# Kernel optimization log

Hardware: AMD Instinct MI355X
Metric: run time of the kernel (lower is better)

The kernel has to match this reference:

```python
import jax, jax.numpy as jnp
import numpy as np

B, T, IN, H, HH, OUT = 512, 512, 6, 64, 128, 8


def setup_inputs() -> dict:
    key = jax.random.key(0)
    ks = jax.random.split(key, 14)
    def lin(k, fan_in, shape):
        s = 1.0 / np.sqrt(fan_in)
        return jax.random.uniform(k, shape, jnp.float32, -s, s)
    return {
        "x": jax.random.normal(ks[0], (B, T, IN), jnp.float32),
        # initial_linear: input_dim -> hidden
        "W_init": lin(ks[1], IN, (IN, H)), "b_init": lin(ks[2], IN, (H,)),
        # vector-field MLP: hidden -> hh -> hh -> hh -> hidden*input
        "W_in": lin(ks[3], H, (H, HH)),  "b_in": lin(ks[4], H, (HH,)),
        "W_h1": lin(ks[5], HH, (HH, HH)), "b_h1": lin(ks[6], HH, (HH,)),
        "W_h2": lin(ks[7], HH, (HH, HH)), "b_h2": lin(ks[8], HH, (HH,)),
        "W_out": lin(ks[9], HH, (HH, H * IN)), "b_out": lin(ks[10], HH, (H * IN,)),
        # final linear: hidden -> output
        "W_fin": lin(ks[11], H, (H, OUT)), "b_fin": lin(ks[12], H, (OUT,)),
    }


def reference(x, W_init, b_init, W_in, b_in, W_h1, b_h1, W_h2, b_h2,
              W_out, b_out, W_fin, b_fin):
    # vector field: f(h) -> (B, H, IN) matrix; dh/dt = f(h) @ dX/dt
    def vf(h, dX):
        z = jax.nn.relu(h @ W_in + b_in)
        z = jax.nn.relu(z @ W_h1 + b_h1)
        z = jax.nn.relu(z @ W_h2 + b_h2)
        A = jnp.tanh(z @ W_out + b_out).reshape(h.shape[0], H, IN)
        return jnp.einsum("bhi,bi->bh", A, dX)

    # h0 from initial value of the path (spline.evaluate(0) == x[:, 0])
    h0 = x[:, 0] @ W_init + b_init  # (B, H)

    # linear interpolation: dX/dt constant on each unit interval
    dX = jnp.swapaxes(x[:, 1:] - x[:, :-1], 0, 1)  # (T-1, B, IN)

    def rk4_step(h, d):
        k1 = vf(h, d)
        k2 = vf(h + 0.5 * k1, d)
        k3 = vf(h + 0.5 * k2, d)
        k4 = vf(h + k3, d)
        h_new = h + (k1 + 2.0 * k2 + 2.0 * k3 + k4) / 6.0
        return h_new, h_new

    _, hs = jax.lax.scan(rk4_step, h0, dX)  # (T-1, B, H)
    hidden = jnp.concatenate([h0[None], hs], axis=0)  # (T, B, H)
    hidden = jnp.swapaxes(hidden, 0, 1)  # (B, T, H)

    # return_sequences=True -> final linear on all steps
    return hidden @ W_fin + b_fin  # (B, T, OUT)
```

## Files before the change

### kernel.cpp

```cpp
#include <hip/hip_runtime.h>
#include <stdint.h>

namespace {

constexpr int B_   = 512;
constexpr int T_   = 512;
constexpr int IN_  = 6;
constexpr int H_   = 64;
constexpr int HH_  = 128;
constexpr int OUT_ = 8;

typedef _Float16 f16x2 __attribute__((ext_vector_type(2)));

__device__ __forceinline__ float dot2f(uint32_t w, uint32_t z, float acc) {
    return __builtin_amdgcn_fdot2(__builtin_bit_cast(f16x2, w),
                                  __builtin_bit_cast(f16x2, z), acc, false);
}

__device__ __forceinline__ uint32_t pack2f(float a, float b) {
    f16x2 p;
    p[0] = (_Float16)a;
    p[1] = (_Float16)b;
    return __builtin_bit_cast(uint32_t, p);
}

__device__ __forceinline__ float pxor1(float v) {
    int y = __builtin_amdgcn_mov_dpp(__builtin_bit_cast(int, v), 0xB1, 0xF, 0xF, true);
    return v + __builtin_bit_cast(float, y);
}

__device__ __forceinline__ float pxor2(float v) {
    int y = __builtin_amdgcn_mov_dpp(__builtin_bit_cast(int, v), 0x4E, 0xF, 0xF, true);
    return v + __builtin_bit_cast(float, y);
}

__device__ __forceinline__ float tanh_fast(float v) {
    float ax = fabsf(v);
    float e  = __expf(2.0f * ax);
    float r  = 1.0f - 2.0f / (e + 1.0f);
    return copysignf(r, v);
}

__global__ __launch_bounds__(256, 2) void cde_kernel(
    const float* __restrict__ x,
    const float* __restrict__ W_init, const float* __restrict__ b_init,
    const float* __restrict__ W_in,   const float* __restrict__ b_in,
    const float* __restrict__ W_h1,   const float* __restrict__ b_h1,
    const float* __restrict__ W_h2,   const float* __restrict__ b_h2,
    const float* __restrict__ W_out,  const float* __restrict__ b_out,
    const float* __restrict__ W_fin,  const float* __restrict__ b_fin,
    float* __restrict__ out)
{
    const int t  = threadIdx.x;
    const int c  = t >> 1;
    const int kh = t & 1;
    const int b  = blockIdx.x;

    __shared__ alignas(16) uint32_t hinu[H_ / 2];
    __shared__ alignas(16) uint32_t zAu[HH_ / 2];
    __shared__ alignas(16) uint32_t zBu[HH_ / 2];
    __shared__ uint32_t w1s[32 * HH_];
    __shared__ float dxs[IN_];
    __shared__ float hbuf[H_];
    __shared__ float wfin_s[H_ * OUT_];
    __shared__ float bfin_s[OUT_];

    uint32_t w2[32], w3[32], w4[96];
    #pragma unroll
    for (int i = 0; i < 32; ++i) {
        int k = kh * 64 + 2 * i;
        w2[i] = pack2f(W_h1[k * HH_ + c], W_h1[(k + 1) * HH_ + c]);
        w3[i] = pack2f(W_h2[k * HH_ + c], W_h2[(k + 1) * HH_ + c]);
    }
    #pragma unroll
    for (int j = 0; j < 3; ++j) {
        const int col = 3 * c + j;
        #pragma unroll
        for (int i = 0; i < 32; ++i) {
            int k = kh * 64 + 2 * i;
            w4[j * 32 + i] = pack2f(W_out[k * 384 + col], W_out[(k + 1) * 384 + col]);
        }
    }
    for (int i = t; i < 32 * HH_; i += 256) {
        int kp = i >> 7, cc = i & 127;
        w1s[i] = pack2f(W_in[(2 * kp) * HH_ + cc], W_in[(2 * kp + 1) * HH_ + cc]);
    }
    for (int i = t; i < H_ * OUT_; i += 256) wfin_s[i] = W_fin[i];
    if (t < OUT_) bfin_s[t] = b_fin[t];

    const float bin_r = b_in[c];
    const float bh1_r = b_h1[c];
    const float bh2_r = b_h2[c];
    float bo[3];
    #pragma unroll
    for (int j = 0; j < 3; ++j) bo[j] = b_out[3 * c + j];
    const int  dbase = (c & 1) * 3;
    const int  r_own = t >> 2;
    const bool wrt   = (t & 3) == 0;

    const size_t xbase = (size_t)b * T_ * IN_;
    const size_t obase = (size_t)b * T_ * OUT_;

    float xa = 0.f, xb = 0.f;
    if (t < IN_) {
        xa = x[xbase + t];
        xb = x[xbase + IN_ + t];
        dxs[t] = xb - xa;
        xa = xb;
        xb = x[xbase + 2 * IN_ + t];
    }

    if (t < H_) {
        float s = b_init[t];
        #pragma unroll
        for (int i = 0; i < IN_; ++i) s += x[xbase + i] * W_init[i * H_ + t];
        hbuf[t] = s;
        ((_Float16*)hinu)[t] = (_Float16)s;
    }
    __syncthreads();

    float h_reg = hbuf[r_own];
    float hacc  = 0.f;

#define OUT_STAGE(TT)                                                          \
    if (t < 64) {                                                              \
        int o_ = t & 7, part_ = t >> 3;                                        \
        float s_ = 0.f;                                                        \
        _Pragma("unroll")                                                      \
        for (int j = 0; j < 8; ++j)                                            \
            s_ += hbuf[part_ * 8 + j] * wfin_s[(part_ * 8 + j) * OUT_ + o_];   \
        s_ += __shfl_xor(s_, 8);                                               \
        s_ += __shfl_xor(s_, 16);                                              \
        s_ += __shfl_xor(s_, 32);                                              \
        if (part_ == 0)                                                        \
            out[obase + (size_t)(TT) * OUT_ + o_] = s_ + bfin_s[o_];           \
    }

    OUT_STAGE(0)

    float dxr[3];

    for (int step = 0; step < T_ - 1; ++step) {
        #pragma unroll
        for (int s4 = 0; s4 < 4; ++s4) {
            if (s4 == 0) {
                #pragma unroll
                for (int j = 0; j < 3; ++j) dxr[j] = dxs[dbase + j];
                if (step > 0) { OUT_STAGE(step) }
            }
            {
                uint32_t hv[16];
                const uint32_t* hp = hinu + kh * 16;
                *(uint4*)&hv[0]  = *(const uint4*)(hp);
                *(uint4*)&hv[4]  = *(const uint4*)(hp + 4);
                *(uint4*)&hv[8]  = *(const uint4*)(hp + 8);
                *(uint4*)&hv[12] = *(const uint4*)(hp + 12);
                const int w1base = (kh * 16) * HH_ + c;
                float a0 = 0.f, a1 = 0.f, a2 = 0.f, a3 = 0.f;
                #pragma unroll
                for (int i = 0; i < 16; ++i) {
                    uint32_t wv = w1s[w1base + i * HH_];
                    if ((i & 3) == 0)      a0 = dot2f(wv, hv[i], a0);
                    else if ((i & 3) == 1) a1 = dot2f(wv, hv[i], a1);
                    else if ((i & 3) == 2) a2 = dot2f(wv, hv[i], a2);
                    else                   a3 = dot2f(wv, hv[i], a3);
                }
                float z = fmaxf(bin_r + pxor1((a0 + a1) + (a2 + a3)), 0.f);
                if (kh == 0) ((_Float16*)zAu)[c] = (_Float16)z;
            }
            __syncthreads();

            {
                uint32_t zv[32];
                const uint32_t* zp = zAu + kh * 32;
                #pragma unroll
                for (int q = 0; q < 8; ++q)
                    *(uint4*)&zv[4 * q] = *(const uint4*)(zp + 4 * q);
                float a0 = 0.f, a1 = 0.f, a2 = 0.f, a3 = 0.f;
                #pragma unroll
                for (int i = 0; i < 32; ++i) {
                    if ((i & 3) == 0)      a0 = dot2f(w2[i], zv[i], a0);
                    else if ((i & 3) == 1) a1 = dot2f(w2[i], zv[i], a1);
                    else if ((i & 3) == 2) a2 = dot2f(w2[i], zv[i], a2);
                    else                   a3 = dot2f(w2[i], zv[i], a3);
                }
                float z = fmaxf(bh1_r + pxor1((a0 + a1) + (a2 + a3)), 0.f);
                if (kh == 0) ((_Float16*)zBu)[c] = (_Float16)z;
            }
            __syncthreads();

            {
                uint32_t zv[32];
                const uint32_t* zp = zBu + kh * 32;
                #pragma unroll
                for (int q = 0; q < 8; ++q)
                    *(uint4*)&zv[4 * q] = *(const uint4*)(zp + 4 * q);
                float a0 = 0.f, a1 = 0.f, a2 = 0.f, a3 = 0.f;
                #pragma unroll
                for (int i = 0; i < 32; ++i) {
                    if ((i & 3) == 0)      a0 = dot2f(w3[i], zv[i], a0);
                    else if ((i & 3) == 1) a1 = dot2f(w3[i], zv[i], a1);
                    else if ((i & 3) == 2) a2 = dot2f(w3[i], zv[i], a2);
                    else                   a3 = dot2f(w3[i], zv[i], a3);
                }
                float z = fmaxf(bh2_r + pxor1((a0 + a1) + (a2 + a3)), 0.f);
                if (kh == 0) ((_Float16*)zAu)[c] = (_Float16)z;
            }
            __syncthreads();

            {
                uint32_t zv[32];
                const uint32_t* zp = zAu + kh * 32;
                #pragma unroll
                for (int q = 0; q < 8; ++q)
                    *(uint4*)&zv[4 * q] = *(const uint4*)(zp + 4 * q);
                float p0 = 0.f, p1 = 0.f, p2 = 0.f, p3 = 0.f, p4 = 0.f, p5 = 0.f;
                #pragma unroll
                for (int i = 0; i < 16; ++i) {
                    uint32_t ze = zv[2 * i], zo = zv[2 * i + 1];
                    p0 = dot2f(w4[2 * i],          ze, p0);
                    p1 = dot2f(w4[2 * i + 1],      zo, p1);
                    p2 = dot2f(w4[32 + 2 * i],     ze, p2);
                    p3 = dot2f(w4[32 + 2 * i + 1], zo, p3);
                    p4 = dot2f(w4[64 + 2 * i],     ze, p4);
                    p5 = dot2f(w4[64 + 2 * i + 1], zo, p5);
                }
                float av0 = bo[0] + pxor1(p0 + p1);
                float av1 = bo[1] + pxor1(p2 + p3);
                float av2 = bo[2] + pxor1(p4 + p5);
                float kvp = tanh_fast(av0) * dxr[0]
                          + tanh_fast(av1) * dxr[1]
                          + tanh_fast(av2) * dxr[2];
                float kv = pxor2(kvp);

                hacc += ((s4 == 1 || s4 == 2) ? 2.0f : 1.0f) * kv;
                float hs;
                if (s4 < 3) {
                    hs = h_reg + ((s4 == 2) ? 1.0f : 0.5f) * kv;
                } else {
                    h_reg += hacc * (1.0f / 6.0f);
                    hacc = 0.f;
                    hs = h_reg;
                }
                if (wrt) {
                    ((_Float16*)hinu)[r_own] = (_Float16)hs;
                    if (s4 == 3) hbuf[r_own] = h_reg;
                }
            }
            if (s4 == 3 && step + 2 < T_ && t < IN_) {
                dxs[t] = xb - xa;
                xa = xb;
                if (step + 3 < T_) xb = x[xbase + (size_t)(step + 3) * IN_ + t];
            }
            __syncthreads();
        }
    }

    OUT_STAGE(T_ - 1)
#undef OUT_STAGE
}

}

extern "C" void kernel_launch(void* const* d_in, const int* in_sizes, int n_in,
                              void* d_out, int out_size, void* d_ws, size_t ws_size,
                              hipStream_t stream) {
    const float* x      = (const float*)d_in[0];
    const float* W_init = (const float*)d_in[1];
    const float* b_init = (const float*)d_in[2];
    const float* W_in   = (const float*)d_in[3];
    const float* b_in   = (const float*)d_in[4];
    const float* W_h1   = (const float*)d_in[5];
    const float* b_h1   = (const float*)d_in[6];
    const float* W_h2   = (const float*)d_in[7];
    const float* b_h2   = (const float*)d_in[8];
    const float* W_out  = (const float*)d_in[9];
    const float* b_out  = (const float*)d_in[10];
    const float* W_fin  = (const float*)d_in[11];
    const float* b_fin  = (const float*)d_in[12];
    float* out = (float*)d_out;

    cde_kernel<<<dim3(B_), dim3(256), 0, stream>>>(
        x, W_init, b_init, W_in, b_in, W_h1, b_h1, W_h2, b_h2,
        W_out, b_out, W_fin, b_fin, out);
}
```

Baseline: 3.229 ms.

## Move hidden-layer weights to padded LDS, keep W_in in registers, disable AGPRs

Moves the W_h1 and W_h2 weight slices out of per-thread registers into padded, row-major LDS tables read with 128-bit loads, and moves W_in from LDS into registers. The goal is to lower VGPR pressure so the 2-blocks-per-CU launch bound fits without spills or AGPR use, and to replace strided scalar LDS reads with vectorized ones. The dot-product chains are rearranged into fewer accumulators that interleave loads with compute, and the W_fin table is padded to 9 columns to reduce bank conflicts. The trade-off is extra LDS traffic for the two 128x128 layers on every RK4 substage, plus longer dependent FMA chains from having fewer accumulators.

```diff
diff --git a/kernel.cpp b/kernel.cpp
--- a/kernel.cpp
+++ b/kernel.cpp
@@ -1,5 +1,15 @@
 #include <hip/hip_runtime.h>
 #include <stdint.h>
+
+#if defined(__has_attribute)
+#if __has_attribute(amdgpu_agpr_alloc)
+#define AGPR0 __attribute__((amdgpu_agpr_alloc(0)))
+#else
+#define AGPR0
+#endif
+#else
+#define AGPR0
+#endif
 
 namespace {
 
@@ -10,6 +20,10 @@
 constexpr int HH_  = 128;
 constexpr int OUT_ = 8;
 
+constexpr int WROW = 36;
+constexpr int WOFF = HH_ * WROW + 16;
+constexpr int WSZ  = WOFF + HH_ * WROW;
+
 typedef _Float16 f16x2 __attribute__((ext_vector_type(2)));
 
 __device__ __forceinline__ float dot2f(uint32_t w, uint32_t z, float acc) {
@@ -28,7 +42,6 @@
     int y = __builtin_amdgcn_mov_dpp(__builtin_bit_cast(int, v), 0xB1, 0xF, 0xF, true);
     return v + __builtin_bit_cast(float, y);
 }
-
 __device__ __forceinline__ float pxor2(float v) {
     int y = __builtin_amdgcn_mov_dpp(__builtin_bit_cast(int, v), 0x4E, 0xF, 0xF, true);
     return v + __builtin_bit_cast(float, y);
@@ -41,7 +54,7 @@
     return copysignf(r, v);
 }
 
-__global__ __launch_bounds__(256, 2) void cde_kernel(
+__global__ AGPR0 __launch_bounds__(256, 2) void cde_kernel(
     const float* __restrict__ x,
     const float* __restrict__ W_init, const float* __restrict__ b_init,
     const float* __restrict__ W_in,   const float* __restrict__ b_in,
@@ -56,21 +69,21 @@
     const int kh = t & 1;
     const int b  = blockIdx.x;
 
+    __shared__ alignas(16) uint32_t w2s[WSZ];
+    __shared__ alignas(16) uint32_t w3s[WSZ];
     __shared__ alignas(16) uint32_t hinu[H_ / 2];
     __shared__ alignas(16) uint32_t zAu[HH_ / 2];
     __shared__ alignas(16) uint32_t zBu[HH_ / 2];
-    __shared__ uint32_t w1s[32 * HH_];
     __shared__ float dxs[IN_];
     __shared__ float hbuf[H_];
-    __shared__ float wfin_s[H_ * OUT_];
+    __shared__ float wfin_s[H_ * 9];
     __shared__ float bfin_s[OUT_];
 
-    uint32_t w2[32], w3[32], w4[96];
+    uint32_t w1[16], w4[96];
     #pragma unroll
-    for (int i = 0; i < 32; ++i) {
-        int k = kh * 64 + 2 * i;
-        w2[i] = pack2f(W_h1[k * HH_ + c], W_h1[(k + 1) * HH_ + c]);
-        w3[i] = pack2f(W_h2[k * HH_ + c], W_h2[(k + 1) * HH_ + c]);
+    for (int i = 0; i < 16; ++i) {
+        int k = kh * 32 + 2 * i;
+        w1[i] = pack2f(W_in[k * HH_ + c], W_in[(k + 1) * HH_ + c]);
     }
     #pragma unroll
     for (int j = 0; j < 3; ++j) {
@@ -81,11 +94,18 @@
             w4[j * 32 + i] = pack2f(W_out[k * 384 + col], W_out[(k + 1) * 384 + col]);
         }
     }
-    for (int i = t; i < 32 * HH_; i += 256) {
-        int kp = i >> 7, cc = i & 127;
-        w1s[i] = pack2f(W_in[(2 * kp) * HH_ + cc], W_in[(2 * kp + 1) * HH_ + cc]);
-    }
-    for (int i = t; i < H_ * OUT_; i += 256) wfin_s[i] = W_fin[i];
+    for (int i = t; i < 2 * HH_ * 32; i += 256) {
+        int khw = i >> 12;
+        int rem = i & 4095;
+        int kp  = rem >> 7;
+        int cc  = rem & 127;
+        int dst = khw * WOFF + cc * WROW + kp;
+        int k   = khw * 64 + 2 * kp;
+        w2s[dst] = pack2f(W_h1[k * HH_ + cc], W_h1[(k + 1) * HH_ + cc]);
+        w3s[dst] = pack2f(W_h2[k * HH_ + cc], W_h2[(k + 1) * HH_ + cc]);
+    }
+    for (int i = t; i < H_ * OUT_; i += 256)
+        wfin_s[(i >> 3) * 9 + (i & 7)] = W_fin[i];
     if (t < OUT_) bfin_s[t] = b_fin[t];
 
     const float bin_r = b_in[c];
@@ -95,8 +115,11 @@
     #pragma unroll
     for (int j = 0; j < 3; ++j) bo[j] = b_out[3 * c + j];
     const int  dbase = (c & 1) * 3;
-    const int  r_own = t >> 2;
+    const int  r_own = c >> 1;
     const bool wrt   = (t & 3) == 0;
+
+    const uint32_t* wp2 = w2s + kh * WOFF + c * WROW;
+    const uint32_t* wp3 = w3s + kh * WOFF + c * WROW;
 
     const size_t xbase = (size_t)b * T_ * IN_;
     const size_t obase = (size_t)b * T_ * OUT_;
@@ -128,7 +151,7 @@
         float s_ = 0.f;                                                        \
         _Pragma("unroll")                                                      \
         for (int j = 0; j < 8; ++j)                                            \
-            s_ += hbuf[part_ * 8 + j] * wfin_s[(part_ * 8 + j) * OUT_ + o_];   \
+            s_ += hbuf[part_ * 8 + j] * wfin_s[(part_ * 8 + j) * 9 + o_];      \
         s_ += __shfl_xor(s_, 8);                                               \
         s_ += __shfl_xor(s_, 16);                                              \
         s_ += __shfl_xor(s_, 32);                                              \
@@ -149,88 +172,147 @@
                 if (step > 0) { OUT_STAGE(step) }
             }
             {
-                uint32_t hv[16];
                 const uint32_t* hp = hinu + kh * 16;
-                *(uint4*)&hv[0]  = *(const uint4*)(hp);
-                *(uint4*)&hv[4]  = *(const uint4*)(hp + 4);
-                *(uint4*)&hv[8]  = *(const uint4*)(hp + 8);
-                *(uint4*)&hv[12] = *(const uint4*)(hp + 12);
-                const int w1base = (kh * 16) * HH_ + c;
-                float a0 = 0.f, a1 = 0.f, a2 = 0.f, a3 = 0.f;
-                #pragma unroll
-                for (int i = 0; i < 16; ++i) {
-                    uint32_t wv = w1s[w1base + i * HH_];
-                    if ((i & 3) == 0)      a0 = dot2f(wv, hv[i], a0);
-                    else if ((i & 3) == 1) a1 = dot2f(wv, hv[i], a1);
-                    else if ((i & 3) == 2) a2 = dot2f(wv, hv[i], a2);
-                    else                   a3 = dot2f(wv, hv[i], a3);
-                }
-                float z = fmaxf(bin_r + pxor1((a0 + a1) + (a2 + a3)), 0.f);
+                uint4 q0 = *reinterpret_cast<const uint4*>(hp);
+                uint4 q1 = *reinterpret_cast<const uint4*>(hp + 4);
+                uint4 q2 = *reinterpret_cast<const uint4*>(hp + 8);
+                uint4 q3 = *reinterpret_cast<const uint4*>(hp + 12);
+                float a = 0.f, d = 0.f;
+                #pragma unroll
+                for (int m = 0; m < 4; ++m) {
+                    a = dot2f(w1[m],      (&q0.x)[m], a);
+                    d = dot2f(w1[4 + m],  (&q1.x)[m], d);
+                    a = dot2f(w1[8 + m],  (&q2.x)[m], a);
+                    d = dot2f(w1[12 + m], (&q3.x)[m], d);
+                }
+                float z = fmaxf(bin_r + pxor1(a + d), 0.f);
                 if (kh == 0) ((_Float16*)zAu)[c] = (_Float16)z;
             }
             __syncthreads();
 
             {
-                uint32_t zv[32];
                 const uint32_t* zp = zAu + kh * 32;
-                #pragma unroll
-                for (int q = 0; q < 8; ++q)
-                    *(uint4*)&zv[4 * q] = *(const uint4*)(zp + 4 * q);
-                float a0 = 0.f, a1 = 0.f, a2 = 0.f, a3 = 0.f;
-                #pragma unroll
-                for (int i = 0; i < 32; ++i) {
-                    if ((i & 3) == 0)      a0 = dot2f(w2[i], zv[i], a0);
-                    else if ((i & 3) == 1) a1 = dot2f(w2[i], zv[i], a1);
-                    else if ((i & 3) == 2) a2 = dot2f(w2[i], zv[i], a2);
-                    else                   a3 = dot2f(w2[i], zv[i], a3);
-                }
-                float z = fmaxf(bh1_r + pxor1((a0 + a1) + (a2 + a3)), 0.f);
+                uint4 z0 = *reinterpret_cast<const uint4*>(zp);
+                uint4 z1 = *reinterpret_cast<const uint4*>(zp + 4);
+                uint4 wa = *reinterpret_cast<const uint4*>(wp2);
+                uint4 wb = *reinterpret_cast<const uint4*>(wp2 + 4);
+                float a = 0.f, d = 0.f;
+                #pragma unroll
+                for (int m = 0; m < 4; ++m) {
+                    a = dot2f((&wa.x)[m], (&z0.x)[m], a);
+                    d = dot2f((&wb.x)[m], (&z1.x)[m], d);
+                }
+                uint4 z2 = *reinterpret_cast<const uint4*>(zp + 8);
+                uint4 z3 = *reinterpret_cast<const uint4*>(zp + 12);
+                uint4 wc = *reinterpret_cast<const uint4*>(wp2 + 8);
+                uint4 wd = *reinterpret_cast<const uint4*>(wp2 + 12);
+                #pragma unroll
+                for (int m = 0; m < 4; ++m) {
+                    a = dot2f((&wc.x)[m], (&z2.x)[m], a);
+                    d = dot2f((&wd.x)[m], (&z3.x)[m], d);
+                }
+                uint4 z4 = *reinterpret_cast<const uint4*>(zp + 16);
+                uint4 z5 = *reinterpret_cast<const uint4*>(zp + 20);
+                uint4 we = *reinterpret_cast<const uint4*>(wp2 + 16);
+                uint4 wf = *reinterpret_cast<const uint4*>(wp2 + 20);
+                #pragma unroll
+                for (int m = 0; m < 4; ++m) {
+                    a = dot2f((&we.x)[m], (&z4.x)[m], a);
+                    d = dot2f((&wf.x)[m], (&z5.x)[m], d);
+                }
+                uint4 z6 = *reinterpret_cast<const uint4*>(zp + 24);
+                uint4 z7 = *reinterpret_cast<const uint4*>(zp + 28);
+                uint4 wg = *reinterpret_cast<const uint4*>(wp2 + 24);
+                uint4 wh = *reinterpret_cast<const uint4*>(wp2 + 28);
+                #pragma unroll
+                for (int m = 0; m < 4; ++m) {
+                    a = dot2f((&wg.x)[m], (&z6.x)[m], a);
+                    d = dot2f((&wh.x)[m], (&z7.x)[m], d);
+                }
+                float z = fmaxf(bh1_r + pxor1(a + d), 0.f);
                 if (kh == 0) ((_Float16*)zBu)[c] = (_Float16)z;
             }
             __syncthreads();
 
             {
-                uint32_t zv[32];
                 const uint32_t* zp = zBu + kh * 32;
-                #pragma unroll
-                for (int q = 0; q < 8; ++q)
-                    *(uint4*)&zv[4 * q] = *(const uint4*)(zp + 4 * q);
-                float a0 = 0.f, a1 = 0.f, a2 = 0.f, a3 = 0.f;
-                #pragma unroll
-                for (int i = 0; i < 32; ++i) {
-                    if ((i & 3) == 0)      a0 = dot2f(w3[i], zv[i], a0);
-                    else if ((i & 3) == 1) a1 = dot2f(w3[i], zv[i], a1);
-                    else if ((i & 3) == 2) a2 = dot2f(w3[i], zv[i], a2);
-                    else                   a3 = dot2f(w3[i], zv[i], a3);
-                }
-                float z = fmaxf(bh2_r + pxor1((a0 + a1) + (a2 + a3)), 0.f);
+                uint4 z0 = *reinterpret_cast<const uint4*>(zp);
+                uint4 z1 = *reinterpret_cast<const uint4*>(zp + 4);
+                uint4 wa = *reinterpret_cast<const uint4*>(wp3);
+                uint4 wb = *reinterpret_cast<const uint4*>(wp3 + 4);
+                float a = 0.f, d = 0.f;
+                #pragma unroll
+                for (int m = 0; m < 4; ++m) {
+                    a = dot2f((&wa.x)[m], (&z0.x)[m], a);
+                    d = dot2f((&wb.x)[m], (&z1.x)[m], d);
+                }
+                uint4 z2 = *reinterpret_cast<const uint4*>(zp + 8);
+                uint4 z3 = *reinterpret_cast<const uint4*>(zp + 12);
+                uint4 wc = *reinterpret_cast<const uint4*>(wp3 + 8);
+                uint4 wd = *reinterpret_cast<const uint4*>(wp3 + 12);
+                #pragma unroll
+                for (int m = 0; m < 4; ++m) {
+                    a = dot2f((&wc.x)[m], (&z2.x)[m], a);
+                    d = dot2f((&wd.x)[m], (&z3.x)[m], d);
+                }
+                uint4 z4 = *reinterpret_cast<const uint4*>(zp + 16);
+                uint4 z5 = *reinterpret_cast<const uint4*>(zp + 20);
+                uint4 we = *reinterpret_cast<const uint4*>(wp3 + 16);
+                uint4 wf = *reinterpret_cast<const uint4*>(wp3 + 20);
+                #pragma unroll
+                for (int m = 0; m < 4; ++m) {
+                    a = dot2f((&we.x)[m], (&z4.x)[m], a);
+                    d = dot2f((&wf.x)[m], (&z5.x)[m], d);
+                }
+                uint4 z6 = *reinterpret_cast<const uint4*>(zp + 24);
+                uint4 z7 = *reinterpret_cast<const uint4*>(zp + 28);
+                uint4 wg = *reinterpret_cast<const uint4*>(wp3 + 24);
+                uint4 wh = *reinterpret_cast<const uint4*>(wp3 + 28);
+                #pragma unroll
+                for (int m = 0; m < 4; ++m) {
+                    a = dot2f((&wg.x)[m], (&z6.x)[m], a);
+                    d = dot2f((&wh.x)[m], (&z7.x)[m], d);
+                }
+                float z = fmaxf(bh2_r + pxor1(a + d), 0.f);
                 if (kh == 0) ((_Float16*)zAu)[c] = (_Float16)z;
             }
             __syncthreads();
 
             {
-                uint32_t zv[32];
                 const uint32_t* zp = zAu + kh * 32;
-                #pragma unroll
-                for (int q = 0; q < 8; ++q)
-                    *(uint4*)&zv[4 * q] = *(const uint4*)(zp + 4 * q);
-                float p0 = 0.f, p1 = 0.f, p2 = 0.f, p3 = 0.f, p4 = 0.f, p5 = 0.f;
-                #pragma unroll
-                for (int i = 0; i < 16; ++i) {
-                    uint32_t ze = zv[2 * i], zo = zv[2 * i + 1];
-                    p0 = dot2f(w4[2 * i],          ze, p0);
-                    p1 = dot2f(w4[2 * i + 1],      zo, p1);
-                    p2 = dot2f(w4[32 + 2 * i],     ze, p2);
-                    p3 = dot2f(w4[32 + 2 * i + 1], zo, p3);
-                    p4 = dot2f(w4[64 + 2 * i],     ze, p4);
-                    p5 = dot2f(w4[64 + 2 * i + 1], zo, p5);
-                }
-                float av0 = bo[0] + pxor1(p0 + p1);
-                float av1 = bo[1] + pxor1(p2 + p3);
-                float av2 = bo[2] + pxor1(p4 + p5);
-                float kvp = tanh_fast(av0) * dxr[0]
-                          + tanh_fast(av1) * dxr[1]
-                          + tanh_fast(av2) * dxr[2];
+                uint4 z0 = *reinterpret_cast<const uint4*>(zp);
+                uint4 z1 = *reinterpret_cast<const uint4*>(zp + 4);
+                uint4 z2 = *reinterpret_cast<const uint4*>(zp + 8);
+                uint4 z3 = *reinterpret_cast<const uint4*>(zp + 12);
+                float av0 = 0.f, av1 = 0.f, av2 = 0.f;
+                #pragma unroll
+                for (int m = 0; m < 4; ++m) {
+                    uint32_t y0 = (&z0.x)[m], y1 = (&z1.x)[m], y2 = (&z2.x)[m], y3 = (&z3.x)[m];
+                    av0 = dot2f(w4[m],      y0, av0); av0 = dot2f(w4[4 + m],  y1, av0);
+                    av0 = dot2f(w4[8 + m],  y2, av0); av0 = dot2f(w4[12 + m], y3, av0);
+                    av1 = dot2f(w4[32 + m],      y0, av1); av1 = dot2f(w4[36 + m], y1, av1);
+                    av1 = dot2f(w4[40 + m],      y2, av1); av1 = dot2f(w4[44 + m], y3, av1);
+                    av2 = dot2f(w4[64 + m],      y0, av2); av2 = dot2f(w4[68 + m], y1, av2);
+                    av2 = dot2f(w4[72 + m],      y2, av2); av2 = dot2f(w4[76 + m], y3, av2);
+                }
+                uint4 z4 = *reinterpret_cast<const uint4*>(zp + 16);
+                uint4 z5 = *reinterpret_cast<const uint4*>(zp + 20);
+                uint4 z6 = *reinterpret_cast<const uint4*>(zp + 24);
+                uint4 z7 = *reinterpret_cast<const uint4*>(zp + 28);
+                #pragma unroll
+                for (int m = 0; m < 4; ++m) {
+                    uint32_t y4 = (&z4.x)[m], y5 = (&z5.x)[m], y6 = (&z6.x)[m], y7 = (&z7.x)[m];
+                    av0 = dot2f(w4[16 + m], y4, av0); av0 = dot2f(w4[20 + m], y5, av0);
+                    av0 = dot2f(w4[24 + m], y6, av0); av0 = dot2f(w4[28 + m], y7, av0);
+                    av1 = dot2f(w4[48 + m], y4, av1); av1 = dot2f(w4[52 + m], y5, av1);
+                    av1 = dot2f(w4[56 + m], y6, av1); av1 = dot2f(w4[60 + m], y7, av1);
+                    av2 = dot2f(w4[80 + m], y4, av2); av2 = dot2f(w4[84 + m], y5, av2);
+                    av2 = dot2f(w4[88 + m], y6, av2); av2 = dot2f(w4[92 + m], y7, av2);
+                }
+                av0 = pxor1(av0); av1 = pxor1(av1); av2 = pxor1(av2);
+                float kvp = tanh_fast(bo[0] + av0) * dxr[0]
+                          + tanh_fast(bo[1] + av1) * dxr[1]
+                          + tanh_fast(bo[2] + av2) * dxr[2];
                 float kv = pxor2(kvp);
 
                 hacc += ((s4 == 1 || s4 == 2) ? 2.0f : 1.0f) * kv;
```

Measured after the change: 3.452 ms. 1.07x slower.
